# Optimization experiments

Measured on AMD Instinct MI355X. Metric: run time of the kernel, lower is better.

## Reference

```python
import jax, jax.numpy as jnp
import numpy as np

SCALE = 32.0  # hardcoded self.scale in the module


def fwht(x):
    """Fast Walsh-Hadamard transform along last dim (power-of-2 length).
    Equivalent to x @ H_n (Sylvester Hadamard), unnormalized."""
    orig_shape = x.shape
    n = orig_shape[-1]
    x = x.reshape(-1, n)
    h = 2
    while h <= n:
        x = x.reshape(-1, n // h, h)
        half = h // 2
        a = x[:, :, :half]
        b = x[:, :, half:]
        x = jnp.concatenate([a + b, a - b], axis=-1)
        h *= 2
    return x.reshape(orig_shape)


def setup_inputs() -> dict:
    key = jax.random.key(0)
    k1, k2, k3, k4, k5 = jax.random.split(key, 5)
    B, S, N, M = 8, 2048, 4096, 4096
    x = jax.random.normal(k1, (B, S, N), dtype=jnp.float32)
    W = jax.random.normal(k2, (M, N), dtype=jnp.float32) * 0.02  # nn.Linear weight [out, in]
    SU = jax.random.uniform(k3, (N,), dtype=jnp.float32, minval=0.5, maxval=1.5)
    SV = jax.random.uniform(k4, (M,), dtype=jnp.float32, minval=0.5, maxval=1.5)
    Wscale = jax.random.uniform(k5, (M,), dtype=jnp.float32, minval=0.5, maxval=1.5)
    return {"x": x, "W": W, "SU": SU, "SV": SV, "Wscale": Wscale}


def reference(x, W, SU, SV, Wscale):
    n = SU.shape[0]
    m = SV.shape[0]
    inv_sqrt_n = 1.0 / np.sqrt(n).astype(np.float32)
    inv_sqrt_m = 1.0 / np.sqrt(m).astype(np.float32)
    h = x.reshape(-1, n) * SU                       # per-channel input scale
    h = fwht(h) * (inv_sqrt_n / SCALE)              # normalized Hadamard rotation / scale
    h = jnp.einsum('tn,mn->tm', h, W) * Wscale      # linear + per-channel weight scale
    h = fwht(h) * inv_sqrt_m                        # inverse (normalized) Hadamard rotation
    h = h * (SV * SCALE)                            # per-channel output scale * scale
    return h.reshape(*x.shape[:-1], m)
```

## Files before the change

### kernel.cpp

```cpp
#include <hip/hip_runtime.h>
#include <hip/hip_bf16.h>

typedef __bf16 bf16x8 __attribute__((ext_vector_type(8)));
typedef float f32x4 __attribute__((ext_vector_type(4)));

__device__ __forceinline__ void gload16(const void* g, void* l) {
  __builtin_amdgcn_global_load_lds(
      (const __attribute__((address_space(1))) void*)g,
      (__attribute__((address_space(3))) void*)l, 16, 0, 0);
}

__device__ __forceinline__ unsigned short f2bf(float f) {
  __hip_bfloat16 h = __float2bfloat16(f);
  union { __hip_bfloat16 h; unsigned short u; } c;
  c.h = h;
  return c.u;
}

__device__ __forceinline__ void fwht16(float v[16]) {
#pragma unroll
  for (int s = 1; s < 16; s <<= 1) {
#pragma unroll
    for (int i = 0; i < 16; i++) {
      if ((i & s) == 0) {
        float a = v[i], b = v[i | s];
        v[i] = a + b;
        v[i | s] = a - b;
      }
    }
  }
}

__global__ __launch_bounds__(256) void fwht1_kernel(
    const float* __restrict__ x, const float* __restrict__ SU,
    unsigned short* __restrict__ H1) {
  __shared__ float lds[256 * 17];
  const int t = threadIdx.x;
  const size_t row = blockIdx.x;
  const float* xr = x + row * 4096;
  float v[16];
#pragma unroll
  for (int n2 = 0; n2 < 16; n2++) {
    int n = n2 * 256 + t;
    v[n2] = xr[n] * SU[n];
  }
  fwht16(v);
  const int n1 = t >> 4, n0 = t & 15;
#pragma unroll
  for (int j2 = 0; j2 < 16; j2++) lds[(j2 * 16 + n1) * 17 + n0] = v[j2];
  __syncthreads();
#pragma unroll
  for (int k = 0; k < 16; k++) v[k] = lds[((t >> 4) * 16 + k) * 17 + (t & 15)];
  fwht16(v);
#pragma unroll
  for (int k = 0; k < 16; k++) lds[((t >> 4) * 16 + k) * 17 + (t & 15)] = v[k];
  __syncthreads();
#pragma unroll
  for (int k = 0; k < 16; k++) v[k] = lds[t * 17 + k];
  fwht16(v);
  const float cst = 1.0f / 2048.0f;
  union { unsigned short u[16]; uint4 q[2]; } o;
#pragma unroll
  for (int k = 0; k < 16; k++) o.u[k] = f2bf(v[k] * cst);
  uint4* dst = (uint4*)(H1 + row * 4096 + (size_t)t * 16);
  dst[0] = o.q[0];
  dst[1] = o.q[1];
}

__global__ __launch_bounds__(256) void convw_kernel(
    const float4* __restrict__ W4, const float* __restrict__ Wscale,
    uint2* __restrict__ Wb4, int total4, int Nq) {
  int i = blockIdx.x * 256 + threadIdx.x;
  if (i >= total4) return;
  float4 w = W4[i];
  float s = Wscale[i / Nq];
  unsigned int lo = (unsigned)f2bf(w.x * s) | ((unsigned)f2bf(w.y * s) << 16);
  unsigned int hi = (unsigned)f2bf(w.z * s) | ((unsigned)f2bf(w.w * s) << 16);
  Wb4[i] = make_uint2(lo, hi);
}


#define BARRIER()                          \
  do {                                     \
    asm volatile("" ::: "memory");         \
    __builtin_amdgcn_s_barrier();          \
    asm volatile("" ::: "memory");         \
  } while (0)
#define GATE2() asm volatile("s_waitcnt vmcnt(2)" ::: "memory")
#define GATE0() asm volatile("s_waitcnt vmcnt(0)" ::: "memory")

__device__ __forceinline__ void stage_half(const unsigned short* __restrict__ g,
                                           unsigned short* l, int tid, int K) {
#pragma unroll
  for (int i = 0; i < 2; i++) {
    int idx = i * 512 + tid;
    int r = idx >> 3;
    int c = (idx & 7) ^ (r & 7);
    gload16(g + (size_t)r * K + c * 8, l + idx * 8);
  }
}

#define STAGE_A(d, hh, kt) \
  stage_half(Abase + (size_t)(hh)*128 * K + (size_t)(kt)*64, &As[d][(hh)*8192], tid, K)
#define STAGE_B(d, hh, kt) \
  stage_half(Bbase + (size_t)(hh)*128 * K + (size_t)(kt)*64, &Bs[d][(hh)*8192], tid, K)

#define LOAD_A(d, h)                                                          \
  {                                                                           \
    _Pragma("unroll") for (int i = 0; i < 4; i++) {                           \
      _Pragma("unroll") for (int ks = 0; ks < 2; ks++) {                      \
        int r = wm * 128 + (h)*64 + i * 16 + fr;                              \
        int kc = ks * 4 + lhi;                                                \
        ah[i][ks] = *(const bf16x8*)&As[d][r * 64 + ((kc ^ (r & 7)) << 3)];   \
      }                                                                       \
    }                                                                         \
  }

#define LOAD_B(d, v, dst)                                                     \
  {                                                                           \
    _Pragma("unroll") for (int j = 0; j < 2; j++) {                           \
      _Pragma("unroll") for (int ks = 0; ks < 2; ks++) {                      \
        int r = wn * 64 + (v)*32 + j * 16 + fr;                               \
        int kc = ks * 4 + lhi;                                                \
        dst[j][ks] = *(const bf16x8*)&Bs[d][r * 64 + ((kc ^ (r & 7)) << 3)];  \
      }                                                                       \
    }                                                                         \
  }

#define MFMA_PH(h, v, bvx)                                                    \
  {                                                                           \
    __builtin_amdgcn_s_setprio(1);                                            \
    _Pragma("unroll") for (int i = 0; i < 4; i++)                             \
      _Pragma("unroll") for (int j = 0; j < 2; j++)                           \
        _Pragma("unroll") for (int ks = 0; ks < 2; ks++)                      \
          acc[(h)*4 + i][(v)*2 + j] = __builtin_amdgcn_mfma_f32_16x16x32_bf16( \
              ah[i][ks], bvx[j][ks], acc[(h)*4 + i][(v)*2 + j], 0, 0, 0);     \
    __builtin_amdgcn_s_setprio(0);                                            \
  }

__global__ __launch_bounds__(512, 2) void gemm8_kernel(
    const unsigned short* __restrict__ A, const unsigned short* __restrict__ B,
    float* __restrict__ C, int M, int K, int NT) {
  __shared__ __align__(16) unsigned short As[2][256 * 64];
  __shared__ __align__(16) unsigned short Bs[2][256 * 64];
  const int nbn = M >> 8;
  const int cpx = gridDim.x >> 3;
  int bid = blockIdx.x;
  bid = (bid & 7) * cpx + (bid >> 3);
  const int brow = (bid / nbn) << 8;
  const int bcol = (bid % nbn) << 8;
  const int tid = threadIdx.x;
  const int lane = tid & 63;
  const int w = tid >> 6;
  const int wm = w >> 2;
  const int wn = w & 3;
  const int fr = lane & 15;
  const int lhi = lane >> 4;

  const unsigned short* Abase = A + (size_t)brow * K;
  const unsigned short* Bbase = B + (size_t)bcol * K;

  f32x4 acc[8][4];
#pragma unroll
  for (int i = 0; i < 8; i++)
#pragma unroll
    for (int j = 0; j < 4; j++) acc[i][j] = (f32x4){0.f, 0.f, 0.f, 0.f};
  bf16x8 ah[4][2], bv0[2][2], bv1[2][2];

  STAGE_A(0, 0, 0);
  STAGE_A(0, 1, 0);
  STAGE_B(0, 0, 0);
  STAGE_B(0, 1, 0);
  STAGE_A(1, 0, 1);

  const int NTT = NT / 2;
#pragma unroll 1
  for (int t = 0; t < NTT; ++t) {
    const bool last = (t == NTT - 1);
    const int u1 = 2 * t + 1, u2 = 2 * t + 2, u3 = 2 * t + 3;
    GATE2();
    BARRIER();
    STAGE_A(1, 1, u1);
    LOAD_A(0, 0);
    LOAD_B(0, 0, bv0);
    MFMA_PH(0, 0, bv0);
    BARRIER();
    STAGE_B(1, 0, u1);
    LOAD_B(0, 1, bv1);
    MFMA_PH(0, 1, bv1);
    BARRIER();
    STAGE_B(1, 1, u1);
    LOAD_A(0, 1);
    MFMA_PH(1, 1, bv1);
    BARRIER();
    if (!last) STAGE_A(0, 0, u2);
    MFMA_PH(1, 0, bv0);
    if (last) { GATE0(); } else { GATE2(); }
    BARRIER();
    if (!last) STAGE_A(0, 1, u2);
    LOAD_A(1, 0);
    LOAD_B(1, 0, bv0);
    MFMA_PH(0, 0, bv0);
    BARRIER();
    if (!last) STAGE_B(0, 0, u2);
    LOAD_B(1, 1, bv1);
    MFMA_PH(0, 1, bv1);
    BARRIER();
    if (!last) STAGE_B(0, 1, u2);
    LOAD_A(1, 1);
    MFMA_PH(1, 1, bv1);
    BARRIER();
    if (!last) STAGE_A(1, 0, u3);
    MFMA_PH(1, 0, bv0);
  }

  const int crow0 = brow + wm * 128 + lhi * 4;
  const int ccol0 = bcol + wn * 64 + fr;
#pragma unroll
  for (int mi = 0; mi < 8; mi++)
#pragma unroll
    for (int nj = 0; nj < 4; nj++)
#pragma unroll
      for (int q = 0; q < 4; q++)
        C[(size_t)(crow0 + mi * 16 + q) * M + ccol0 + nj * 16] = acc[mi][nj][q];
}

__global__ __launch_bounds__(256) void fwht2_kernel(
    float* __restrict__ Y, const float* __restrict__ SV) {
  __shared__ float lds[256 * 17];
  const int t = threadIdx.x;
  const size_t row = blockIdx.x;
  float* yr = Y + row * 4096;
  float v[16];
#pragma unroll
  for (int n2 = 0; n2 < 16; n2++) v[n2] = yr[n2 * 256 + t];
  fwht16(v);
  const int n1 = t >> 4, n0 = t & 15;
#pragma unroll
  for (int j2 = 0; j2 < 16; j2++) lds[(j2 * 16 + n1) * 17 + n0] = v[j2];
  __syncthreads();
#pragma unroll
  for (int k = 0; k < 16; k++) v[k] = lds[((t >> 4) * 16 + k) * 17 + (t & 15)];
  fwht16(v);
#pragma unroll
  for (int k = 0; k < 16; k++) lds[((t >> 4) * 16 + k) * 17 + (t & 15)] = v[k];
  __syncthreads();
#pragma unroll
  for (int k = 0; k < 16; k++) v[k] = lds[t * 17 + k];
  fwht16(v);
  float outv[16];
#pragma unroll
  for (int k = 0; k < 16; k++) outv[k] = v[k] * 0.5f * SV[(size_t)t * 16 + k];
  float4* dst = (float4*)(yr + (size_t)t * 16);
#pragma unroll
  for (int k = 0; k < 4; k++)
    dst[k] = make_float4(outv[4 * k], outv[4 * k + 1], outv[4 * k + 2],
                         outv[4 * k + 3]);
}

extern "C" void kernel_launch(void* const* d_in, const int* in_sizes, int n_in,
                              void* d_out, int out_size, void* d_ws,
                              size_t ws_size, hipStream_t stream) {
  const float* x = (const float*)d_in[0];
  const float* W = (const float*)d_in[1];
  const float* SU = (const float*)d_in[2];
  const float* SV = (const float*)d_in[3];
  const float* Wscale = (const float*)d_in[4];
  const int N = in_sizes[2];
  const int M = in_sizes[3];
  const int T = in_sizes[0] / N;

  unsigned short* H1 = (unsigned short*)d_ws;
  unsigned short* Wb = H1 + (size_t)T * N;
  float* out = (float*)d_out;

  fwht1_kernel<<<T, 256, 0, stream>>>(x, SU, H1);
  const int total4 = (int)(((long)M * N) / 4);
  convw_kernel<<<(total4 + 255) / 256, 256, 0, stream>>>(
      (const float4*)W, Wscale, (uint2*)Wb, total4, N / 4);
  const int NT = N / 64;
  gemm8_kernel<<<(T / 256) * (M / 256), 512, 0, stream>>>(H1, Wb, out, M, N, NT);
  fwht2_kernel<<<T, 256, 0, stream>>>(out, SV);
}
```

Measured before the change: 806.8 us.

## Restructure GEMM main loop into ping-pong phases with explicit LDS waits and barriers

Reorders the bf16 GEMM main loop so LDS fragment reads are issued before the global-to-LDS stage copies, with explicit lgkmcnt waits and extra barriers separating load phases from MFMA phases. Memory clobbers on barriers are replaced by sched_barrier fences around the vmcnt waits. The aim is to overlap LDS reads and global prefetches with MFMA work in a ping-pong style across waves. It adds barriers, and removing the memory clobbers risks the compiler reordering LDS accesses across the barriers.

Measured after the change: 758.9 us. -5.9%, faster.

```diff
diff --git a/kernel.cpp b/kernel.cpp
--- a/kernel.cpp
+++ b/kernel.cpp
@@ -80,14 +80,22 @@
 }
 
 
-#define BARRIER()                          \
-  do {                                     \
-    asm volatile("" ::: "memory");         \
-    __builtin_amdgcn_s_barrier();          \
-    asm volatile("" ::: "memory");         \
+#define BAR() __builtin_amdgcn_s_barrier()
+#define SCHED() __builtin_amdgcn_sched_barrier(0)
+#define GATE2()                              \
+  do {                                       \
+    SCHED();                                 \
+    asm volatile("s_waitcnt vmcnt(2)");      \
+    SCHED();                                 \
   } while (0)
-#define GATE2() asm volatile("s_waitcnt vmcnt(2)" ::: "memory")
-#define GATE0() asm volatile("s_waitcnt vmcnt(0)" ::: "memory")
+#define GATE0()                              \
+  do {                                       \
+    SCHED();                                 \
+    asm volatile("s_waitcnt vmcnt(0)");      \
+    SCHED();                                 \
+  } while (0)
+#define LGKM0() asm volatile("s_waitcnt lgkmcnt(0)")
+#define LGKM8() asm volatile("s_waitcnt lgkmcnt(8)")
 
 __device__ __forceinline__ void stage_half(const unsigned short* __restrict__ g,
                                            unsigned short* l, int tid, int K) {
@@ -105,11 +113,11 @@
 #define STAGE_B(d, hh, kt) \
   stage_half(Bbase + (size_t)(hh)*128 * K + (size_t)(kt)*64, &Bs[d][(hh)*8192], tid, K)
 
-#define LOAD_A(d, h)                                                          \
+#define LOAD_A(d, m)                                                          \
   {                                                                           \
     _Pragma("unroll") for (int i = 0; i < 4; i++) {                           \
       _Pragma("unroll") for (int ks = 0; ks < 2; ks++) {                      \
-        int r = wm * 128 + (h)*64 + i * 16 + fr;                              \
+        int r = wm * 128 + (m)*64 + i * 16 + fr;                              \
         int kc = ks * 4 + lhi;                                                \
         ah[i][ks] = *(const bf16x8*)&As[d][r * 64 + ((kc ^ (r & 7)) << 3)];   \
       }                                                                       \
@@ -127,14 +135,14 @@
     }                                                                         \
   }
 
-#define MFMA_PH(h, v, bvx)                                                    \
+#define MFMA_PH(m, v, bvx)                                                    \
   {                                                                           \
     __builtin_amdgcn_s_setprio(1);                                            \
     _Pragma("unroll") for (int i = 0; i < 4; i++)                             \
       _Pragma("unroll") for (int j = 0; j < 2; j++)                           \
         _Pragma("unroll") for (int ks = 0; ks < 2; ks++)                      \
-          acc[(h)*4 + i][(v)*2 + j] = __builtin_amdgcn_mfma_f32_16x16x32_bf16( \
-              ah[i][ks], bvx[j][ks], acc[(h)*4 + i][(v)*2 + j], 0, 0, 0);     \
+          acc[(m)*4 + i][(v)*2 + j] = __builtin_amdgcn_mfma_f32_16x16x32_bf16( \
+              ah[i][ks], bvx[j][ks], acc[(m)*4 + i][(v)*2 + j], 0, 0, 0);     \
     __builtin_amdgcn_s_setprio(0);                                            \
   }
 
@@ -172,46 +180,70 @@
   STAGE_B(0, 0, 0);
   STAGE_B(0, 1, 0);
   STAGE_A(1, 0, 1);
+  GATE2();
+  BAR();
 
   const int NTT = NT / 2;
 #pragma unroll 1
   for (int t = 0; t < NTT; ++t) {
     const bool last = (t == NTT - 1);
     const int u1 = 2 * t + 1, u2 = 2 * t + 2, u3 = 2 * t + 3;
-    GATE2();
-    BARRIER();
-    STAGE_A(1, 1, u1);
     LOAD_A(0, 0);
     LOAD_B(0, 0, bv0);
+    STAGE_A(1, 1, u1);
+    LGKM8();
+    BAR();
+    LGKM0();
     MFMA_PH(0, 0, bv0);
-    BARRIER();
+    BAR();
+    LOAD_B(0, 1, bv1);
     STAGE_B(1, 0, u1);
-    LOAD_B(0, 1, bv1);
+    BAR();
+    LGKM0();
     MFMA_PH(0, 1, bv1);
-    BARRIER();
+    BAR();
+    LOAD_A(0, 1);
     STAGE_B(1, 1, u1);
-    LOAD_A(0, 1);
+    BAR();
+    LGKM0();
     MFMA_PH(1, 1, bv1);
-    BARRIER();
-    if (!last) STAGE_A(0, 0, u2);
+    BAR();
+    if (!last) {
+      STAGE_A(0, 0, u2);
+      GATE2();
+    } else {
+      GATE0();
+    }
+    BAR();
     MFMA_PH(1, 0, bv0);
-    if (last) { GATE0(); } else { GATE2(); }
-    BARRIER();
-    if (!last) STAGE_A(0, 1, u2);
+    BAR();
     LOAD_A(1, 0);
     LOAD_B(1, 0, bv0);
+    if (!last) STAGE_A(0, 1, u2);
+    LGKM8();
+    BAR();
+    LGKM0();
     MFMA_PH(0, 0, bv0);
-    BARRIER();
+    BAR();
+    LOAD_B(1, 1, bv1);
     if (!last) STAGE_B(0, 0, u2);
-    LOAD_B(1, 1, bv1);
+    BAR();
+    LGKM0();
     MFMA_PH(0, 1, bv1);
-    BARRIER();
+    BAR();
+    LOAD_A(1, 1);
     if (!last) STAGE_B(0, 1, u2);
-    LOAD_A(1, 1);
+    BAR();
+    LGKM0();
     MFMA_PH(1, 1, bv1);
-    BARRIER();
-    if (!last) STAGE_A(1, 0, u3);
+    BAR();
+    if (!last) {
+      STAGE_A(1, 0, u3);
+      GATE2();
+    }
+    BAR();
     MFMA_PH(1, 0, bv0);
+    BAR();
   }
 
   const int crow0 = brow + wm * 128 + lhi * 4;
```
